# Kernel tuning notes

Hardware: AMD Instinct MI355X
Metric: run time of the kernel (lower is better)

The kernel has to match this reference:

```python
import jax, jax.numpy as jnp
import numpy as np
from jax import lax

KH = KW = 3
K = KH * KW
STRIDE = 1
PAD = 1
DIL = 1
GN_GROUPS = 32
EPS = 1e-5


def setup_inputs() -> dict:
    key = jax.random.key(0)
    k0, k1, k2 = jax.random.split(key, 3)
    B, C, H, W = 8, 256, 64, 64
    O = 256
    x = jax.random.normal(k0, (B, C, H, W), jnp.float32)
    # offset-predicting conv (DeformConv2dPack.conv_offset); small weights keep offsets ~O(1)
    w_off = jax.random.normal(k1, (2 * K, C, KH, KW), jnp.float32) * 0.01
    b_off = jnp.zeros((2 * K,), jnp.float32)
    w_dcn = jax.random.normal(k2, (O, C, KH, KW), jnp.float32) * (1.0 / np.sqrt(C * K))
    gamma = jnp.ones((O,), jnp.float32)
    beta = jnp.zeros((O,), jnp.float32)
    return {"x": x, "w_off": w_off, "b_off": b_off, "w_dcn": w_dcn, "gamma": gamma, "beta": beta}


def _deform_conv(x, w_off, b_off, w_dcn):
    B, C, H, W = x.shape
    O = w_dcn.shape[0]
    # offsets via standard conv: [B, 2K, Ho, Wo]; channel layout (k, (dy, dx))
    offset = lax.conv_general_dilated(
        x, w_off, (STRIDE, STRIDE), [(PAD, PAD), (PAD, PAD)],
        rhs_dilation=(DIL, DIL), dimension_numbers=("NCHW", "OIHW", "NCHW"))
    offset = offset + b_off[None, :, None, None]
    Ho, Wo = offset.shape[2], offset.shape[3]
    off = offset.reshape(B, K, 2, Ho, Wo)
    ky = jnp.repeat(jnp.arange(KH), KW)  # [K]
    kx = jnp.tile(jnp.arange(KW), KH)    # [K]
    base_y = (jnp.arange(Ho) * STRIDE - PAD)[None, :, None] + (ky * DIL)[:, None, None]  # [K,Ho,1]
    base_x = (jnp.arange(Wo) * STRIDE - PAD)[None, None, :] + (kx * DIL)[:, None, None]  # [K,1,Wo]
    py = off[:, :, 0] + base_y[None].astype(off.dtype)  # [B,K,Ho,Wo]
    px = off[:, :, 1] + base_x[None].astype(off.dtype)

    def sample_one(xi, py_i, px_i):  # xi [C,H,W]; py/px [K,Ho,Wo]
        y0 = jnp.floor(py_i)
        x0 = jnp.floor(px_i)
        dy = py_i - y0
        dx = px_i - x0
        y0i = y0.astype(jnp.int32)
        x0i = x0.astype(jnp.int32)

        def gather(yi, xj, w):
            valid = (yi >= 0) & (yi < H) & (xj >= 0) & (xj < W)
            yc = jnp.clip(yi, 0, H - 1)
            xc = jnp.clip(xj, 0, W - 1)
            return xi[:, yc, xc] * (w * valid)[None]  # [C,K,Ho,Wo]

        return (gather(y0i, x0i, (1 - dy) * (1 - dx))
                + gather(y0i, x0i + 1, (1 - dy) * dx)
                + gather(y0i + 1, x0i, dy * (1 - dx))
                + gather(y0i + 1, x0i + 1, dy * dx))

    cols = jax.vmap(sample_one)(x, py, px)  # [B,C,K,Ho,Wo]
    y = jnp.einsum("ock,bckp->bop", w_dcn.reshape(O, C, K),
                   cols.reshape(B, C, K, Ho * Wo))
    return y.reshape(B, O, Ho, Wo)


def _group_norm(y, gamma, beta):
    B, O, Ho, Wo = y.shape
    g = y.reshape(B, GN_GROUPS, O // GN_GROUPS, Ho, Wo)
    mean = g.mean(axis=(2, 3, 4), keepdims=True)
    var = g.var(axis=(2, 3, 4), keepdims=True)
    yn = ((g - mean) * lax.rsqrt(var + EPS)).reshape(B, O, Ho, Wo)
    return yn * gamma[None, :, None, None] + beta[None, :, None, None]


def reference(x, w_off, b_off, w_dcn, gamma, beta):
    y = _deform_conv(x, w_off, b_off, w_dcn)
    y = _group_norm(y, gamma, beta)
    return y * jnp.tanh(jax.nn.softplus(y))  # Mish
```

## Files before the change

kernel.cpp:

```cpp
#include <hip/hip_runtime.h>
#include <hip/hip_bf16.h>
#include <math.h>

typedef __bf16 bf16x8 __attribute__((ext_vector_type(8)));
typedef float f32x4 __attribute__((ext_vector_type(4)));
typedef float f32x2 __attribute__((ext_vector_type(2)));
typedef unsigned int u32;
typedef u32 u32x4 __attribute__((ext_vector_type(4)));
typedef u32 u32x2 __attribute__((ext_vector_type(2)));


#define FENCE() __builtin_amdgcn_sched_barrier(0)
#define VMCNT(n) do { asm volatile("s_waitcnt vmcnt(" #n ")" ::: "memory"); FENCE(); } while (0)
#define LGKM0() do { asm volatile("s_waitcnt lgkmcnt(0)" ::: "memory"); FENCE(); } while (0)

__device__ inline u32 pack2bf16(float a, float b) {
  u32 ua = __float_as_uint(a);
  u32 ub = __float_as_uint(b);
  ua += 0x7fffu + ((ua >> 16) & 1u);
  ub += 0x7fffu + ((ub >> 16) & 1u);
  return (ua >> 16) | (ub & 0xffff0000u);
}

__global__ void prep(const float* __restrict__ w_dcn, const float* __restrict__ w_off,
                     unsigned short* __restrict__ wT4, unsigned short* __restrict__ wOffT,
                     float* __restrict__ stats) {
  size_t id = (size_t)blockIdx.x * 256 + threadIdx.x;
  if (id < 589824) {
    int o  = (int)(id / 2304);
    int ck = (int)(id % 2304);
    int k = ck >> 8, c = ck & 255;
    float v = w_dcn[(size_t)(o * 256 + c) * 9 + k];
    u32 uv = __float_as_uint(v);
    uv += 0x7fffu + ((uv >> 16) & 1u);
    int tile = ck >> 6, kk = ck & 63;
    int lin = o * 128 + kk * 2;
    int swz = lin ^ ((o & 7) << 4);
    *(unsigned short*)((char*)wT4 + (size_t)tile * 32768 + swz) = (unsigned short)(uv >> 16);
  } else if (id < 663552) {
    int r = (int)(id - 589824);
    int tile = r >> 11;
    int rr = r & 2047;
    int o = rr >> 6, kk = rr & 63;
    int k = tile >> 2, cc = tile & 3;
    int c = (cc << 6) + kk;
    float v = (o < 18) ? w_off[(size_t)(o * 256 + c) * 9 + k] : 0.f;
    u32 uv = __float_as_uint(v);
    uv += 0x7fffu + ((uv >> 16) & 1u);
    int swz = (o * 128 + kk * 2) ^ ((o & 7) << 4);
    *(unsigned short*)((char*)wOffT + (size_t)tile * 4096 + swz) = (unsigned short)(uv >> 16);
  } else if (id < 664064) {
    stats[id - 663552] = 0.f;
  }
}

__global__ __launch_bounds__(256) void transpose_x(const float* __restrict__ x,
                                                   unsigned short* __restrict__ xT) {
  __shared__ float tl[64][65];
  int bx = blockIdx.x;
  int b = bx >> 8;
  int y = (bx >> 2) & 63;
  int cb = (bx & 3) << 6;
  int t = threadIdx.x;
  int xi = t & 63, cr = t >> 6;
  size_t base = (((size_t)(b * 256 + cb) * 64 + y) << 6);
#pragma unroll
  for (int rep = 0; rep < 16; ++rep) {
    int cl = rep * 4 + cr;
    tl[cl][xi] = x[base + (size_t)cl * 4096 + xi];
  }
  __syncthreads();
  int xw = t & 63, cpair = t >> 6;
#pragma unroll
  for (int r = 0; r < 2; ++r) {
    int cgl = cpair * 2 + r;
    int cg = (cb >> 3) + cgl;
    u32 pk4[4];
#pragma unroll
    for (int i = 0; i < 4; ++i)
      pk4[i] = pack2bf16(tl[cgl * 8 + 2 * i][xw], tl[cgl * 8 + 2 * i + 1][xw]);
    u32x4 v = {pk4[0], pk4[1], pk4[2], pk4[3]};
    *(u32x4*)((char*)xT + (((size_t)b << 21)) + ((size_t)cg << 16) + ((y << 6) + xw) * 16) = v;
  }
}

__global__ __launch_bounds__(256) void conv_offset_mfma(
    const unsigned short* __restrict__ xT, const unsigned short* __restrict__ wOffT,
    float* __restrict__ offs) {
  __shared__ union {
    unsigned short Bo[4][2][2048];
    float red[4][64][32];
  } sm;
  const int bx = blockIdx.x;
  const int lb = ((bx & 7) << 6) + (bx >> 3);
  const int b = lb >> 6;
  const int row = lb & 63;
  const int t = threadIdx.x;
  const int lane = t & 63, w = t >> 6;
  const char* xTbB = (const char*)xT + ((size_t)b << 21);

  f32x4 acc[4][2];
#pragma unroll
  for (int i = 0; i < 4; ++i)
#pragma unroll
    for (int j = 0; j < 2; ++j) {
      f32x4 z = {0.f, 0.f, 0.f, 0.f};
      acc[i][j] = z;
    }

  auto stageB = [&](int k, int d) {
    const char* src = (const char*)wOffT + ((size_t)((k << 2) + w) << 12);
    char* dstb = (char*)&sm.Bo[w][d][0];
#pragma unroll
    for (int i2 = 0; i2 < 4; ++i2) {
      __builtin_amdgcn_global_load_lds(
          (const __attribute__((address_space(1))) u32*)(src + (i2 << 10) + (lane << 4)),
          (__attribute__((address_space(3))) u32*)(dstb + (i2 << 10)),
          16, 0, 0);
    }
  };

  stageB(0, 0);
  u32x4 rA[8];
  const u32x4 zv = {0u, 0u, 0u, 0u};

  for (int k = 0; k < 9; ++k) {
    int ky = k / 3, kxv = k - ky * 3;
    int rowp = row - 1 + ky;
    bool rok = ((unsigned)rowp < 64u);
    bool ok[4];
    if (rok) {
      int pix[4];
#pragma unroll
      for (int pg = 0; pg < 4; ++pg) {
        int xs = (pg << 4) + (lane & 15) + kxv - 1;
        ok[pg] = ((unsigned)xs < 64u);
        int xc = min(max(xs, 0), 63);
        pix[pg] = (rowp << 6) + xc;
      }
#pragma unroll
      for (int s = 0; s < 2; ++s) {
        const char* base = xTbB + ((size_t)((w << 3) + (s << 2) + (lane >> 4)) << 16);
#pragma unroll
        for (int pg = 0; pg < 4; ++pg)
          rA[s * 4 + pg] = *(const u32x4*)(base + ((size_t)pix[pg] << 4));
      }
    }
    if (k < 8) stageB(k + 1, (k + 1) & 1);
    VMCNT(4);
    if (rok) {
      const char* Bb = (const char*)&sm.Bo[w][k & 1][0];
#pragma unroll
      for (int s = 0; s < 2; ++s) {
        bf16x8 bb[2];
        int kx = (s << 6) + ((lane >> 4) << 4);
#pragma unroll
        for (int j = 0; j < 2; ++j) {
          int o = (j << 4) + (lane & 15);
          bb[j] = *(const bf16x8*)(Bb + o * 128 + (kx ^ ((o & 7) << 4)));
        }
#pragma unroll
        for (int pg = 0; pg < 4; ++pg) {
          u32x4 av = ok[pg] ? rA[s * 4 + pg] : zv;
          bf16x8 af = __builtin_bit_cast(bf16x8, av);
#pragma unroll
          for (int j = 0; j < 2; ++j)
            acc[pg][j] = __builtin_amdgcn_mfma_f32_16x16x32_bf16(af, bb[j], acc[pg][j], 0, 0, 0);
        }
      }
    }
  }

#pragma unroll
  for (int pg = 0; pg < 4; ++pg)
#pragma unroll
    for (int j = 0; j < 2; ++j)
#pragma unroll
      for (int r = 0; r < 4; ++r) {
        int px = (pg << 4) + ((lane >> 4) << 2) + r;
        int o = (j << 4) + (lane & 15);
        sm.red[w][px][o] = acc[pg][j][r];
      }
  __syncthreads();
  {
    int px = t >> 2, oq = (t & 3) << 3;
#pragma unroll
    for (int e = 0; e < 8; ++e) {
      int o = oq + e;
      if (o < 18) {
        float sv = sm.red[0][px][o] + sm.red[1][px][o]
                 + sm.red[2][px][o] + sm.red[3][px][o];
        offs[((size_t)b * 4096 + (row << 6) + px) * 18 + o] = sv;
      }
    }
  }
}

union ArenaM {
  struct {
    unsigned short A[2][128][64];
    unsigned short Bt[3][16384];
  } m;
  unsigned short ytile[256][136];
};

__global__ __launch_bounds__(512) void dcn_main(
    const unsigned short* __restrict__ xT, const float* __restrict__ offs,
    const float* __restrict__ boff, const unsigned short* __restrict__ wT4,
    unsigned short* __restrict__ yb, float* __restrict__ stats) {
  __shared__ ArenaM ar;
  __shared__ u32 pcor[9][128][2];
  __shared__ float pwt[9][128][4];

  const int bx = blockIdx.x;
  const int lb = ((bx & 7) << 5) + (bx >> 3);
  const int b = lb >> 5;
  const int pxbase = (lb & 31) << 7;
  const int t = threadIdx.x;
  const int lane = t & 63, wid = t >> 6;
  const char* xTbB = (const char*)xT + ((size_t)b << 21);
  const int pxs = ((wid & 1) << 6) + lane;
  const int gp = (wid >> 1) << 1;
  const int wr = wid >> 2, wc = wid & 3;
  const int obase = wc << 6;

  for (int idx = t; idx < 1152; idx += 512) {
    int k = idx >> 7, px = idx & 127;
    int pxg = pxbase + px;
    int yy = pxg >> 6, xx = pxg & 63;
    int ky = k / 3, kx = k - ky * 3;
    const float* op = offs + ((size_t)b * 4096 + pxg) * 18 + k * 2;
    float py = op[0] + boff[k * 2] + (float)(yy - 1 + ky);
    float pxf = op[1] + boff[k * 2 + 1] + (float)(xx - 1 + kx);
    float fy = floorf(py), fx = floorf(pxf);
    float dy = py - fy, dx = pxf - fx;
    int y0 = (int)fy, x0 = (int)fx;
    int y1 = y0 + 1, x1 = x0 + 1;
    float vy0 = ((unsigned)y0 < 64u) ? 1.f : 0.f;
    float vy1 = ((unsigned)y1 < 64u) ? 1.f : 0.f;
    float vx0 = ((unsigned)x0 < 64u) ? 1.f : 0.f;
    float vx1 = ((unsigned)x1 < 64u) ? 1.f : 0.f;
    int y0c = min(max(y0, 0), 63), y1c = min(max(y1, 0), 63);
    int x0c = min(max(x0, 0), 63), x1c = min(max(x1, 0), 63);
    pcor[k][px][0] = (u32)((y0c << 6) + x0c) | ((u32)((y0c << 6) + x1c) << 16);
    pcor[k][px][1] = (u32)((y1c << 6) + x0c) | ((u32)((y1c << 6) + x1c) << 16);
    pwt[k][px][0] = (1.f - dy) * (1.f - dx) * vy0 * vx0;
    pwt[k][px][1] = (1.f - dy) * dx * vy0 * vx1;
    pwt[k][px][2] = dy * (1.f - dx) * vy1 * vx0;
    pwt[k][px][3] = dy * dx * vy1 * vx1;
  }

  f32x4 acc[4][4];
#pragma unroll
  for (int i = 0; i < 4; ++i)
#pragma unroll
    for (int j = 0; j < 4; ++j) {
      f32x4 z = {0.f, 0.f, 0.f, 0.f};
      acc[i][j] = z;
    }

  __syncthreads();

  u32x4 rA[8];

  auto issueA = [&](int tt) {
    int k = tt >> 2, cc = tt & 3;
    u32 c01 = pcor[k][pxs][0], c23 = pcor[k][pxs][1];
    const char* p0 = xTbB + ((size_t)((cc << 3) + gp) << 16);
#pragma unroll
    for (int g = 0; g < 2; ++g) {
      const char* bgp = p0 + ((size_t)g << 16);
      rA[g * 4 + 0] = *(const u32x4*)(bgp + ((size_t)(c01 & 0xffffu) << 4));
      rA[g * 4 + 1] = *(const u32x4*)(bgp + ((size_t)(c01 >> 16) << 4));
      rA[g * 4 + 2] = *(const u32x4*)(bgp + ((size_t)(c23 & 0xffffu) << 4));
      rA[g * 4 + 3] = *(const u32x4*)(bgp + ((size_t)(c23 >> 16) << 4));
    }
  };
  auto issueB = [&](int tt, int bufi) {
    const char* src = (const char*)wT4 + ((size_t)tt << 15) + (wid << 12);
    char* dstb = (char*)&ar.m.Bt[bufi][0] + (wid << 12);
#pragma unroll
    for (int i2 = 0; i2 < 4; ++i2) {
      __builtin_amdgcn_global_load_lds(
          (const __attribute__((address_space(1))) u32*)(src + (i2 << 10) + (lane << 4)),
          (__attribute__((address_space(3))) u32*)(dstb + (i2 << 10)),
          16, 0, 0);
    }
  };
  auto blendA = [&](int tt) {
    int k = tt >> 2;
    f32x4 w = *(const f32x4*)&pwt[k][pxs][0];
    char* dst = (char*)&ar.m.A[tt & 1][0][0] + pxs * 128;
    int sw = (pxs & 7) << 4;
#pragma unroll
    for (int g = 0; g < 2; ++g) {
      u32 o4[4];
#pragma unroll
      for (int e = 0; e < 4; ++e) {
        u32 u0 = rA[g * 4 + 0][e], u1 = rA[g * 4 + 1][e];
        u32 u2 = rA[g * 4 + 2][e], u3 = rA[g * 4 + 3][e];
        float lo = w[0] * __uint_as_float(u0 << 16);
        lo = fmaf(w[1], __uint_as_float(u1 << 16), lo);
        lo = fmaf(w[2], __uint_as_float(u2 << 16), lo);
        lo = fmaf(w[3], __uint_as_float(u3 << 16), lo);
        float hi = w[0] * __uint_as_float(u0 & 0xffff0000u);
        hi = fmaf(w[1], __uint_as_float(u1 & 0xffff0000u), hi);
        hi = fmaf(w[2], __uint_as_float(u2 & 0xffff0000u), hi);
        hi = fmaf(w[3], __uint_as_float(u3 & 0xffff0000u), hi);
        asm("v_cvt_pk_bf16_f32 %0, %1, %2" : "=v"(o4[e]) : "v"(lo), "v"(hi));
      }
      u32x4 ov = {o4[0], o4[1], o4[2], o4[3]};
      *(u32x4*)(dst + (((gp + g) << 4) ^ sw)) = ov;
    }
  };

  issueA(0); FENCE();
  issueB(0, 0); FENCE();
  VMCNT(4);
  blendA(0);
  FENCE();
  issueA(1); FENCE();
  issueB(1, 1); FENCE();
  VMCNT(12);
  LGKM0();
  __builtin_amdgcn_s_barrier();
  FENCE();

  int bm3 = 0;
  for (int tt = 0; tt < 36; ++tt) {
    if (tt < 35) { VMCNT(4); }
    {
      const char* Ab = (const char*)&ar.m.A[tt & 1][0][0];
      const char* Bb = (const char*)&ar.m.Bt[bm3][0];
      __builtin_amdgcn_s_setprio(1);
#pragma unroll
      for (int s = 0; s < 2; ++s) {
        int kx = (s << 6) + ((lane >> 4) << 4);
        bf16x8 a[4], bb[4];
#pragma unroll
        for (int i = 0; i < 4; ++i) {
          int r16 = (wr << 6) + (i << 4) + (lane & 15);
          a[i] = *(const bf16x8*)(Ab + r16 * 128 + (kx ^ ((r16 & 7) << 4)));
        }
#pragma unroll
        for (int j = 0; j < 4; ++j) {
          int o = obase + (j << 4) + (lane & 15);
          bb[j] = *(const bf16x8*)(Bb + o * 128 + (kx ^ ((o & 7) << 4)));
        }
#pragma unroll
        for (int i = 0; i < 4; ++i)
#pragma unroll
          for (int j = 0; j < 4; ++j)
            acc[i][j] = __builtin_amdgcn_mfma_f32_16x16x32_bf16(a[i], bb[j], acc[i][j], 0, 0, 0);
      }
      if (tt < 35) blendA(tt + 1);
      __builtin_amdgcn_s_setprio(0);
    }
    FENCE();
    if (tt < 34) {
      issueA(tt + 2); FENCE();
      int bn = bm3 + 2; if (bn >= 3) bn -= 3;
      issueB(tt + 2, bn); FENCE();
    }
    if (tt == 34) { VMCNT(0); }
    else { VMCNT(12); }
    LGKM0();
    __builtin_amdgcn_s_barrier();
    FENCE();
    bm3 = (bm3 == 2) ? 0 : bm3 + 1;
  }

#pragma unroll
  for (int j = 0; j < 4; ++j) {
    float s1 = 0.f, s2 = 0.f;
#pragma unroll
    for (int i = 0; i < 4; ++i)
#pragma unroll
      for (int r = 0; r < 4; ++r) {
        float v = acc[i][j][r];
        s1 += v;
        s2 += v * v;
      }
    s1 += __shfl_xor(s1, 1, 64);  s2 += __shfl_xor(s2, 1, 64);
    s1 += __shfl_xor(s1, 2, 64);  s2 += __shfl_xor(s2, 2, 64);
    s1 += __shfl_xor(s1, 4, 64);  s2 += __shfl_xor(s2, 4, 64);
    s1 += __shfl_xor(s1, 16, 64); s2 += __shfl_xor(s2, 16, 64);
    s1 += __shfl_xor(s1, 32, 64); s2 += __shfl_xor(s2, 32, 64);
    if ((lane & 0x37) == 0) {
      int g = (obase + (j << 4) + (lane & 15)) >> 3;
      atomicAdd(&stats[((b << 5) + g) * 2 + 0], s1);
      atomicAdd(&stats[((b << 5) + g) * 2 + 1], s2);
    }
  }

#pragma unroll
  for (int i = 0; i < 4; ++i)
#pragma unroll
    for (int j = 0; j < 4; ++j) {
      int o = obase + (j << 4) + (lane & 15);
      int pxr = (wr << 6) + (i << 4) + ((lane >> 4) << 2);
      u32 wv0, wv1;
      asm("v_cvt_pk_bf16_f32 %0, %1, %2" : "=v"(wv0) : "v"(acc[i][j][0]), "v"(acc[i][j][1]));
      asm("v_cvt_pk_bf16_f32 %0, %1, %2" : "=v"(wv1) : "v"(acc[i][j][2]), "v"(acc[i][j][3]));
      u32x2 wv = {wv0, wv1};
      *(u32x2*)((char*)ar.ytile + o * 272 + pxr * 2) = wv;
    }
  __syncthreads();
  {
    int o = t >> 1, half = t & 1;
    const char* srcb = (const char*)ar.ytile + o * 272 + (half << 7);
    unsigned short* dst = yb + (((size_t)(b * 256 + o)) << 12) + pxbase + (half << 6);
#pragma unroll
    for (int qq = 0; qq < 8; ++qq)
      *(u32x4*)((char*)dst + (qq << 4)) = *(const u32x4*)(srcb + (qq << 4));
  }
}

__global__ __launch_bounds__(256) void gn_mish(const unsigned short* __restrict__ yb,
                                               const float* __restrict__ stats,
                                               const float* __restrict__ gamma,
                                               const float* __restrict__ beta,
                                               float* __restrict__ out) {
  int v = blockIdx.x * 512 + threadIdx.x;
#pragma unroll
  for (int it = 0; it < 2; ++it, v += 256) {
    int o = (v >> 9) & 255;
    int b = v >> 17;
    float s1 = stats[((b << 5) + (o >> 3)) * 2 + 0];
    float s2 = stats[((b << 5) + (o >> 3)) * 2 + 1];
    float mean = s1 * (1.f / 32768.f);
    float var = s2 * (1.f / 32768.f) - mean * mean;
    float rstd = rsqrtf(var + 1e-5f);
    float ga = gamma[o] * rstd, be = beta[o] - mean * gamma[o] * rstd;
    u32x4 u = *(const u32x4*)(yb + ((size_t)v << 3));
    float res[8];
#pragma unroll
    for (int e = 0; e < 4; ++e) {
      float va = __uint_as_float(u[e] << 16);
      float vb = __uint_as_float(u[e] & 0xffff0000u);
      float v0 = fmaf(va, ga, be);
      float v1 = fmaf(vb, ga, be);
      float e0 = expf(fminf(v0, 15.f));
      float e1 = expf(fminf(v1, 15.f));
      float n0 = e0 * (e0 + 2.f);
      float n1 = e1 * (e1 + 2.f);
      float m0 = v0 * (n0 / (n0 + 2.f));
      float m1 = v1 * (n1 / (n1 + 2.f));
      if (v0 > 15.f) m0 = v0;
      if (v1 > 15.f) m1 = v1;
      res[2 * e] = m0;
      res[2 * e + 1] = m1;
    }
    f32x4 o0 = {res[0], res[1], res[2], res[3]};
    f32x4 o1 = {res[4], res[5], res[6], res[7]};
    float* dst = out + ((size_t)v << 3);
    *(f32x4*)dst = o0;
    *((f32x4*)dst + 1) = o1;
  }
}

extern "C" void kernel_launch(void* const* d_in, const int* in_sizes, int n_in,
                              void* d_out, int out_size, void* d_ws, size_t ws_size,
                              hipStream_t stream) {
  const float* x     = (const float*)d_in[0];
  const float* w_off = (const float*)d_in[1];
  const float* b_off = (const float*)d_in[2];
  const float* w_dcn = (const float*)d_in[3];
  const float* gamma = (const float*)d_in[4];
  const float* beta  = (const float*)d_in[5];
  float* out = (float*)d_out;
  char* ws = (char*)d_ws;
  unsigned short* xT   = (unsigned short*)(ws);
  unsigned short* yb   = (unsigned short*)(ws + 16777216);
  float* offs          = (float*)(ws + 33554432);
  unsigned short* wT4  = (unsigned short*)(ws + 35913728);
  unsigned short* wOffT= (unsigned short*)(ws + 37093376);
  float* stats         = (float*)(ws + 37240832);
  prep<<<dim3(2594), dim3(256), 0, stream>>>(w_dcn, w_off, wT4, wOffT, stats);
  transpose_x<<<dim3(2048), dim3(256), 0, stream>>>(x, xT);
  conv_offset_mfma<<<dim3(512), dim3(256), 0, stream>>>(xT, wOffT, offs);
  dcn_main<<<dim3(256), dim3(512), 0, stream>>>(xT, offs, b_off, wT4, yb, stats);
  gn_mish<<<dim3(2048), dim3(256), 0, stream>>>(yb, stats, gamma, beta, out);
}
```

Before: 112.2 us.

## Load DCN weight fragments directly into registers instead of staging through LDS

The prep kernel now writes the DCN weights in a per-wave MFMA fragment layout, so each lane can load its B operands with plain 16-byte global loads into a double-buffered register array. This replaces the triple-buffered LDS staging via global_load_lds and the LDS reads of B inside the main loop. The loop is unrolled by two so the register buffer index is a compile-time constant, and the wait counts are adjusted to match. In exchange, the kernel uses many more VGPRs (64 extra dwords for B), which could cut occupancy or cause spills, and each wave fetches its own weights from L2 without sharing them through LDS.

```diff
diff --git a/kernel.cpp b/kernel.cpp
--- a/kernel.cpp
+++ b/kernel.cpp
@@ -4,7 +4,6 @@
 
 typedef __bf16 bf16x8 __attribute__((ext_vector_type(8)));
 typedef float f32x4 __attribute__((ext_vector_type(4)));
-typedef float f32x2 __attribute__((ext_vector_type(2)));
 typedef unsigned int u32;
 typedef u32 u32x4 __attribute__((ext_vector_type(4)));
 typedef u32 u32x2 __attribute__((ext_vector_type(2)));
@@ -34,9 +33,12 @@
     u32 uv = __float_as_uint(v);
     uv += 0x7fffu + ((uv >> 16) & 1u);
     int tile = ck >> 6, kk = ck & 63;
-    int lin = o * 128 + kk * 2;
-    int swz = lin ^ ((o & 7) << 4);
-    *(unsigned short*)((char*)wT4 + (size_t)tile * 32768 + swz) = (unsigned short)(uv >> 16);
+    int wc = o >> 6, j = (o >> 4) & 3, l15 = o & 15;
+    int s = kk >> 5, lhi = (kk >> 3) & 3, e = kk & 7;
+    int lane = (lhi << 4) + l15;
+    int f = (s << 2) + j;
+    size_t off = (size_t)((((tile << 2) + wc) << 3) + f) * 1024 + lane * 16 + e * 2;
+    *(unsigned short*)((char*)wT4 + off) = (unsigned short)(uv >> 16);
   } else if (id < 663552) {
     int r = (int)(id - 589824);
     int tile = r >> 11;
@@ -199,7 +201,6 @@
 union ArenaM {
   struct {
     unsigned short A[2][128][64];
-    unsigned short Bt[3][16384];
   } m;
   unsigned short ytile[256][136];
 };
@@ -262,6 +263,7 @@
   __syncthreads();
 
   u32x4 rA[8];
+  u32x4 Breg[2][8];
 
   auto issueA = [&](int tt) {
     int k = tt >> 2, cc = tt & 3;
@@ -276,16 +278,11 @@
       rA[g * 4 + 3] = *(const u32x4*)(bgp + ((size_t)(c23 >> 16) << 4));
     }
   };
-  auto issueB = [&](int tt, int bufi) {
-    const char* src = (const char*)wT4 + ((size_t)tt << 15) + (wid << 12);
-    char* dstb = (char*)&ar.m.Bt[bufi][0] + (wid << 12);
-#pragma unroll
-    for (int i2 = 0; i2 < 4; ++i2) {
-      __builtin_amdgcn_global_load_lds(
-          (const __attribute__((address_space(1))) u32*)(src + (i2 << 10) + (lane << 4)),
-          (__attribute__((address_space(3))) u32*)(dstb + (i2 << 10)),
-          16, 0, 0);
-    }
+  auto issueB = [&](int tt, int hp2) {
+    const char* src = (const char*)wT4 + ((size_t)(((tt << 2) + wc)) << 13) + ((size_t)lane << 4);
+#pragma unroll
+    for (int f = 0; f < 8; ++f)
+      Breg[hp2][f] = *(const u32x4*)(src + (f << 10));
   };
   auto blendA = [&](int tt) {
     int k = tt >> 2;
@@ -316,58 +313,52 @@
 
   issueA(0); FENCE();
   issueB(0, 0); FENCE();
-  VMCNT(4);
+  VMCNT(8);
   blendA(0);
   FENCE();
   issueA(1); FENCE();
   issueB(1, 1); FENCE();
-  VMCNT(12);
   LGKM0();
   __builtin_amdgcn_s_barrier();
   FENCE();
 
-  int bm3 = 0;
-  for (int tt = 0; tt < 36; ++tt) {
-    if (tt < 35) { VMCNT(4); }
-    {
-      const char* Ab = (const char*)&ar.m.A[tt & 1][0][0];
-      const char* Bb = (const char*)&ar.m.Bt[bm3][0];
-      __builtin_amdgcn_s_setprio(1);
-#pragma unroll
-      for (int s = 0; s < 2; ++s) {
-        int kx = (s << 6) + ((lane >> 4) << 4);
-        bf16x8 a[4], bb[4];
-#pragma unroll
-        for (int i = 0; i < 4; ++i) {
-          int r16 = (wr << 6) + (i << 4) + (lane & 15);
-          a[i] = *(const bf16x8*)(Ab + r16 * 128 + (kx ^ ((r16 & 7) << 4)));
+  for (int tp = 0; tp < 18; ++tp) {
+#pragma unroll
+    for (int hp = 0; hp < 2; ++hp) {
+      const int tt = (tp << 1) + hp;
+      if (tt == 35) { VMCNT(0); } else { VMCNT(8); }
+      {
+        const char* Ab = (const char*)&ar.m.A[hp][0][0];
+        __builtin_amdgcn_s_setprio(1);
+#pragma unroll
+        for (int s = 0; s < 2; ++s) {
+          int kx = (s << 6) + ((lane >> 4) << 4);
+          bf16x8 a[4];
+#pragma unroll
+          for (int i = 0; i < 4; ++i) {
+            int r16 = (wr << 6) + (i << 4) + (lane & 15);
+            a[i] = *(const bf16x8*)(Ab + r16 * 128 + (kx ^ ((r16 & 7) << 4)));
+          }
+#pragma unroll
+          for (int i = 0; i < 4; ++i)
+#pragma unroll
+            for (int j = 0; j < 4; ++j) {
+              bf16x8 bb = __builtin_bit_cast(bf16x8, Breg[hp][(s << 2) + j]);
+              acc[i][j] = __builtin_amdgcn_mfma_f32_16x16x32_bf16(a[i], bb, acc[i][j], 0, 0, 0);
+            }
         }
-#pragma unroll
-        for (int j = 0; j < 4; ++j) {
-          int o = obase + (j << 4) + (lane & 15);
-          bb[j] = *(const bf16x8*)(Bb + o * 128 + (kx ^ ((o & 7) << 4)));
-        }
-#pragma unroll
-        for (int i = 0; i < 4; ++i)
-#pragma unroll
-          for (int j = 0; j < 4; ++j)
-            acc[i][j] = __builtin_amdgcn_mfma_f32_16x16x32_bf16(a[i], bb[j], acc[i][j], 0, 0, 0);
-      }
-      if (tt < 35) blendA(tt + 1);
-      __builtin_amdgcn_s_setprio(0);
-    }
-    FENCE();
-    if (tt < 34) {
-      issueA(tt + 2); FENCE();
-      int bn = bm3 + 2; if (bn >= 3) bn -= 3;
-      issueB(tt + 2, bn); FENCE();
-    }
-    if (tt == 34) { VMCNT(0); }
-    else { VMCNT(12); }
-    LGKM0();
-    __builtin_amdgcn_s_barrier();
-    FENCE();
-    bm3 = (bm3 == 2) ? 0 : bm3 + 1;
+        if (tt < 35) blendA(tt + 1);
+        __builtin_amdgcn_s_setprio(0);
+      }
+      FENCE();
+      if (tt < 34) {
+        issueA(tt + 2); FENCE();
+        issueB(tt + 2, hp); FENCE();
+      }
+      LGKM0();
+      __builtin_amdgcn_s_barrier();
+      FENCE();
+    }
   }
 
 #pragma unroll
```

After: 117.2 us. 1.04x slower.
